# Optimization experiments

Measured on AMD Instinct MI355X. Metric: run time of the kernel, lower is better.

## Reference

```python
import jax, jax.numpy as jnp
import numpy as np

B, E, LC, LE, D = 32, 8, 256, 512, 256   # batch, evi_num, claim_len, evidence_len, emb_dim
OUT, H = 128, 1                          # attention hidden dim, head_num
NEG = -1e18


def setup_inputs() -> dict:
    key = jax.random.key(0)
    ks = jax.random.split(key, 8)
    claim = jax.random.normal(ks[0], (B, E, LC, D), jnp.float32)
    evidence = jax.random.normal(ks[1], (B, E, LE, D), jnp.float32)
    claim_len_mask = jax.random.randint(ks[2], (B, E, 1, LC), 0, 2).astype(jnp.int32)
    evidence_len_mask = jax.random.randint(ks[3], (B, E, 1, LE), 0, 2).astype(jnp.int32)
    s2d = 1.0 / np.sqrt(2 * D)
    so = 1.0 / np.sqrt(OUT)
    W1 = jax.random.normal(ks[4], (2 * D, OUT), jnp.float32) * s2d  # torch W1.weight.T
    w2 = jax.random.normal(ks[5], (OUT, H), jnp.float32) * so
    W2 = jax.random.normal(ks[6], (2 * D, OUT), jnp.float32) * s2d
    w1 = jax.random.normal(ks[7], (OUT, H), jnp.float32) * so
    return {"claim": claim, "claim_len_mask": claim_len_mask,
            "evidence": evidence, "evidence_len_mask": evidence_len_mask,
            "W1": W1, "w2": w2, "W2": W2, "w1": w1}


def _pooled_attend(seq, seq_mask, pooled, W, w):
    # seq: (B,E,L,D), pooled: (B,E,1,D), W: (2D,OUT), w: (OUT,H)
    # cat([seq, pooled_expanded]) @ W  ==  seq @ W[:D] + pooled @ W[D:]  (broadcast)
    h = jnp.tanh(seq @ W[:D] + pooled @ W[D:])          # (B,E,L,OUT)
    att = h @ w                                          # (B,E,L,H)
    mask = jnp.swapaxes(seq_mask, -1, -2).astype(bool)   # (B,E,L,1), broadcast over H
    att = jnp.where(mask, att, NEG)
    scores = jax.nn.softmax(att, axis=-2)                # softmax over L
    out = jnp.einsum('belh,beld->behd', scores, seq)     # (B,E,H,D)
    return out.reshape(out.shape[0], out.shape[1], 1, -1)  # (B,E,1,H*D)


def reference(claim, claim_len_mask, evidence, evidence_len_mask, W1, w2, W2, w1):
    c_mean = jnp.mean(claim, axis=-2, keepdims=True)     # (B,E,1,D)
    e_hat = _pooled_attend(evidence, evidence_len_mask, c_mean, W1, w2)
    e_mean = jnp.mean(evidence, axis=-2, keepdims=True)  # (B,E,1,D)
    c_hat = _pooled_attend(claim, claim_len_mask, e_mean, W2, w1)
    return c_hat, e_hat
```

## Files before the change

kernel.cpp:

```cpp
#include <hip/hip_runtime.h>
#include <hip/hip_bf16.h>
#include <math.h>

#define BE   256
#define DIM  256
#define OUTD 128
#define LCL  256
#define LEV  512
#define NEGV -1e18f

typedef short  bf16x8  __attribute__((ext_vector_type(8)));
typedef float  floatx4 __attribute__((ext_vector_type(4)));

union BF1 { __hip_bfloat16 h; unsigned short u; };
union BF2 { __hip_bfloat162 h; unsigned int u; };

__device__ __forceinline__ float fast_tanh(float x) {
    float xc = fminf(fmaxf(x, -15.f), 15.f);
    float e = __expf(2.f * xc);
    return (e - 1.f) * __builtin_amdgcn_rcpf(e + 1.f);
}

__global__ __launch_bounds__(256) void k_zero(float* __restrict__ a) {
    a[blockIdx.x * 256 + threadIdx.x] = 0.f;
}

__global__ __launch_bounds__(256) void k_pmean(
    const float* __restrict__ claim, const float* __restrict__ evidence,
    float* __restrict__ cmean, float* __restrict__ emean)
{
    const int pair = blockIdx.x;
    const int ch = blockIdx.y;
    const int t = threadIdx.x;
    const float* src;
    float* dst;
    if (ch < 8) { src = claim + ((size_t)pair * LCL + ch * 32) * DIM; dst = cmean + pair * DIM; }
    else        { src = evidence + ((size_t)pair * LEV + (ch - 8) * 32) * DIM; dst = emean + pair * DIM; }
    float s = 0.f;
#pragma unroll
    for (int r = 0; r < 32; ++r) s += src[r * DIM + t];
    unsafeAtomicAdd(&dst[t], s);
}

__global__ __launch_bounds__(256) void k_biasgemm(
    const float* __restrict__ cmean, const float* __restrict__ emean,
    const float* __restrict__ W1, const float* __restrict__ W2,
    float* __restrict__ bias_e, float* __restrict__ bias_c)
{
    const int pair = blockIdx.x;
    const int t = threadIdx.x;
    __shared__ float smc[DIM], sme[DIM];
    smc[t] = cmean[pair * DIM + t] * (1.f / LCL);
    sme[t] = emean[pair * DIM + t] * (1.f / LEV);
    __syncthreads();
    if (t < OUTD) {
        float b = 0.f;
        for (int d = 0; d < DIM; ++d) b += smc[d] * W1[(DIM + d) * OUTD + t];
        bias_e[pair * OUTD + t] = b;
    } else {
        const int o = t - OUTD;
        float b = 0.f;
        for (int d = 0; d < DIM; ++d) b += sme[d] * W2[(DIM + d) * OUTD + o];
        bias_c[pair * OUTD + o] = b;
    }
}

__global__ __launch_bounds__(256) void k_prepW(
    const float* __restrict__ W1, const float* __restrict__ W2,
    unsigned short* __restrict__ WT1, unsigned short* __restrict__ WT2)
{
    const int n = blockIdx.x;
    const float* W = blockIdx.y ? W2 : W1;
    unsigned short* WT = blockIdx.y ? WT2 : WT1;
    const int k = threadIdx.x;
    BF1 c; c.h = __float2bfloat16(W[(size_t)k * OUTD + n]);
    WT[n * DIM + k] = c.u;
}

template <int L>
__global__ __launch_bounds__(256) void k_att(
    const float* __restrict__ seq, const unsigned short* __restrict__ WT,
    const float* __restrict__ wvec, const float* __restrict__ bias,
    float* __restrict__ att)
{
    constexpr int SAPC = 136;
    __shared__ unsigned short sA[128 * SAPC];
    __shared__ float sred[128][2];

    const int pair = blockIdx.x;
    const int rowbase = blockIdx.y * 128;
    const int t = threadIdx.x;
    const int lane = t & 63;
    const int wv = t >> 6;
    const int wrow = wv >> 1, wcolg = wv & 1;
    const int q = lane >> 4, c16 = lane & 15;

    const float4* sp4 = (const float4*)(seq + ((size_t)pair * L + rowbase) * DIM);

    floatx4 acc[4][4];
#pragma unroll
    for (int ra = 0; ra < 4; ++ra)
#pragma unroll
        for (int ct = 0; ct < 4; ++ct) acc[ra][ct] = (floatx4){0.f, 0.f, 0.f, 0.f};

    const unsigned short* wbase = WT + (size_t)(wcolg * 64 + c16) * DIM + q * 8;
    bf16x8 bcur[4], bnxt[4];
#pragma unroll
    for (int ct = 0; ct < 4; ++ct)
        bcur[ct] = *(const bf16x8*)(wbase + ct * 16 * DIM);

    for (int kc = 0; kc < 2; ++kc) {
        __syncthreads();
#pragma unroll
        for (int i = 0; i < 16; ++i) {
            const int idx = t + i * 256;
            const int row = idx >> 5;
            const int f4 = idx & 31;
            const float4 v = sp4[row * 64 + kc * 32 + f4];
            BF2 lo, hi;
            lo.h = __float22bfloat162_rn(make_float2(v.x, v.y));
            hi.h = __float22bfloat162_rn(make_float2(v.z, v.w));
            *(uint2*)&sA[row * SAPC + f4 * 4] = make_uint2(lo.u, hi.u);
        }
        __syncthreads();
#pragma unroll
        for (int ks4 = 0; ks4 < 4; ++ks4) {
            const int ks = kc * 4 + ks4;
            if (ks < 7) {
#pragma unroll
                for (int ct = 0; ct < 4; ++ct)
                    bnxt[ct] = *(const bf16x8*)(wbase + ct * 16 * DIM + (ks + 1) * 32);
            }
            bf16x8 af[4];
#pragma unroll
            for (int ra = 0; ra < 4; ++ra)
                af[ra] = *(const bf16x8*)&sA[(wrow * 64 + ra * 16 + c16) * SAPC + ks4 * 32 + q * 8];
#pragma unroll
            for (int ra = 0; ra < 4; ++ra)
#pragma unroll
                for (int ct = 0; ct < 4; ++ct)
                    acc[ra][ct] = __builtin_amdgcn_mfma_f32_16x16x32_bf16(af[ra], bcur[ct], acc[ra][ct], 0, 0, 0);
#pragma unroll
            for (int ct = 0; ct < 4; ++ct) bcur[ct] = bnxt[ct];
        }
    }

    float bc[4], wc[4];
#pragma unroll
    for (int ct = 0; ct < 4; ++ct) {
        const int col = wcolg * 64 + ct * 16 + c16;
        bc[ct] = bias[pair * OUTD + col];
        wc[ct] = wvec[col];
    }
#pragma unroll
    for (int ra = 0; ra < 4; ++ra) {
#pragma unroll
        for (int reg = 0; reg < 4; ++reg) {
            float s = 0.f;
#pragma unroll
            for (int ct = 0; ct < 4; ++ct)
                s += fast_tanh(acc[ra][ct][reg] + bc[ct]) * wc[ct];
#pragma unroll
            for (int off = 1; off < 16; off <<= 1) s += __shfl_xor(s, off, 64);
            if (c16 == 0)
                sred[wrow * 64 + ra * 16 + q * 4 + reg][wcolg] = s;
        }
    }
    __syncthreads();
    if (t < 128)
        att[(size_t)pair * L + rowbase + t] = sred[t][0] + sred[t][1];
}

template <int L>
__global__ __launch_bounds__(1024) void k_soft(
    const float* __restrict__ seq, const int* __restrict__ mask,
    const float* __restrict__ att, float* __restrict__ outp)
{
    const int pair = blockIdx.x;
    const int t = threadIdx.x;
    __shared__ float p[L];
    __shared__ float red[8];
    __shared__ float red2[4][DIM];

    float lmax = -INFINITY;
    if (t < 256) {
#pragma unroll
        for (int k = 0; k < L / 256; ++k) {
            const int i = t + k * 256;
            float a = att[(size_t)pair * L + i];
            a = mask[pair * L + i] ? a : NEGV;
            p[i] = a;
            lmax = fmaxf(lmax, a);
        }
#pragma unroll
        for (int off = 32; off > 0; off >>= 1) lmax = fmaxf(lmax, __shfl_xor(lmax, off, 64));
        if ((t & 63) == 0) red[t >> 6] = lmax;
    }
    __syncthreads();
    if (t < 256) {
        const float gmax = fmaxf(fmaxf(red[0], red[1]), fmaxf(red[2], red[3]));
        float lsum = 0.f;
#pragma unroll
        for (int k = 0; k < L / 256; ++k) {
            const int i = t + k * 256;
            const float e = expf(p[i] - gmax);
            p[i] = e;
            lsum += e;
        }
#pragma unroll
        for (int off = 32; off > 0; off >>= 1) lsum += __shfl_xor(lsum, off, 64);
        if ((t & 63) == 0) red[4 + (t >> 6)] = lsum;
    }
    __syncthreads();

    const int d = t & 255, lg = t >> 8;
    constexpr int L4 = L / 4;
    const float* sp = seq + (size_t)pair * L * DIM + d;
    float o = 0.f;
    for (int l = lg * L4; l < (lg + 1) * L4; ++l) o += p[l] * sp[(size_t)l * DIM];
    red2[lg][d] = o;
    __syncthreads();
    if (t < 256) {
        const float inv = 1.f / (red[4] + red[5] + red[6] + red[7]);
        outp[pair * DIM + t] = (red2[0][t] + red2[1][t] + red2[2][t] + red2[3][t]) * inv;
    }
}

extern "C" void kernel_launch(void* const* d_in, const int* in_sizes, int n_in,
                              void* d_out, int out_size, void* d_ws, size_t ws_size,
                              hipStream_t stream) {
    const float* claim    = (const float*)d_in[0];
    const int*   cmask    = (const int*)  d_in[1];
    const float* evidence = (const float*)d_in[2];
    const int*   emask    = (const int*)  d_in[3];
    const float* W1       = (const float*)d_in[4];
    const float* w2       = (const float*)d_in[5];
    const float* W2       = (const float*)d_in[6];
    const float* w1       = (const float*)d_in[7];
    float* out = (float*)d_out;

    float* ws = (float*)d_ws;
    float* cmean  = ws;
    float* emean  = cmean + BE * DIM;
    float* bias_e = emean + BE * DIM;
    float* bias_c = bias_e + BE * OUTD;
    float* att_e  = bias_c + BE * OUTD;
    float* att_c  = att_e + BE * LEV;
    unsigned short* WT1 = (unsigned short*)(att_c + BE * LCL);
    unsigned short* WT2 = WT1 + OUTD * DIM;

    k_zero<<<512, 256, 0, stream>>>(cmean);
    k_prepW<<<dim3(128, 2), 256, 0, stream>>>(W1, W2, WT1, WT2);
    k_pmean<<<dim3(BE, 24), 256, 0, stream>>>(claim, evidence, cmean, emean);
    k_biasgemm<<<BE, 256, 0, stream>>>(cmean, emean, W1, W2, bias_e, bias_c);
    k_att<LEV><<<dim3(BE, 4), 256, 0, stream>>>(evidence, WT1, w2, bias_e, att_e);
    k_att<LCL><<<dim3(BE, 2), 256, 0, stream>>>(claim, WT2, w1, bias_c, att_c);
    k_soft<LEV><<<BE, 1024, 0, stream>>>(evidence, emask, att_e, out + BE * DIM);
    k_soft<LCL><<<BE, 1024, 0, stream>>>(claim, cmask, att_c, out);
}
```

Measured before the change: 359.1 us.

## Fuse mean/weight-prep kernels, drop atomics, vectorize softmax weighted sum

Merges the zero, weight-transpose and partial-mean kernels into one launch that writes per-chunk partial sums instead of atomically accumulating. A new reduce-and-bias kernel folds the partials and splits the bias GEMV over 512 threads. The softmax weighted-sum stage now uses float4 loads over 16 row groups with a 16-way shared reduction. Together these cut launch count and atomic traffic and widen memory accesses, at the cost of a larger partial-sum workspace.

```diff
diff --git a/kernel.cpp b/kernel.cpp
--- a/kernel.cpp
+++ b/kernel.cpp
@@ -21,60 +21,73 @@
     return (e - 1.f) * __builtin_amdgcn_rcpf(e + 1.f);
 }
 
-__global__ __launch_bounds__(256) void k_zero(float* __restrict__ a) {
-    a[blockIdx.x * 256 + threadIdx.x] = 0.f;
-}
-
-__global__ __launch_bounds__(256) void k_pmean(
+__global__ __launch_bounds__(256) void k_meanprep(
     const float* __restrict__ claim, const float* __restrict__ evidence,
-    float* __restrict__ cmean, float* __restrict__ emean)
-{
-    const int pair = blockIdx.x;
-    const int ch = blockIdx.y;
-    const int t = threadIdx.x;
-    const float* src;
-    float* dst;
-    if (ch < 8) { src = claim + ((size_t)pair * LCL + ch * 32) * DIM; dst = cmean + pair * DIM; }
-    else        { src = evidence + ((size_t)pair * LEV + (ch - 8) * 32) * DIM; dst = emean + pair * DIM; }
+    const float* __restrict__ W1, const float* __restrict__ W2,
+    float* __restrict__ partial,
+    unsigned short* __restrict__ WT1, unsigned short* __restrict__ WT2)
+{
+    const int b = blockIdx.x;
+    const int t = threadIdx.x;
+    if (b >= 3072) {
+        const int idx = b - 3072;
+        const int side = idx >> 7;
+        const int n = idx & 127;
+        const float* W = side ? W2 : W1;
+        unsigned short* WT = side ? WT2 : WT1;
+        BF1 c; c.h = __float2bfloat16(W[(size_t)t * OUTD + n]);
+        WT[n * DIM + t] = c.u;
+        return;
+    }
+    const int pair = b / 12;
+    const int chunk = b % 12;
+    const float* src = (chunk < 4)
+        ? claim + ((size_t)pair * LCL + chunk * 64) * DIM
+        : evidence + ((size_t)pair * LEV + (chunk - 4) * 64) * DIM;
     float s = 0.f;
 #pragma unroll
-    for (int r = 0; r < 32; ++r) s += src[r * DIM + t];
-    unsafeAtomicAdd(&dst[t], s);
-}
-
-__global__ __launch_bounds__(256) void k_biasgemm(
-    const float* __restrict__ cmean, const float* __restrict__ emean,
+    for (int r = 0; r < 64; ++r) s += src[r * DIM + t];
+    partial[(size_t)b * DIM + t] = s;
+}
+
+__global__ __launch_bounds__(512) void k_redbias(
+    const float* __restrict__ partial,
     const float* __restrict__ W1, const float* __restrict__ W2,
     float* __restrict__ bias_e, float* __restrict__ bias_c)
 {
     const int pair = blockIdx.x;
     const int t = threadIdx.x;
-    __shared__ float smc[DIM], sme[DIM];
-    smc[t] = cmean[pair * DIM + t] * (1.f / LCL);
-    sme[t] = emean[pair * DIM + t] * (1.f / LEV);
-    __syncthreads();
-    if (t < OUTD) {
-        float b = 0.f;
-        for (int d = 0; d < DIM; ++d) b += smc[d] * W1[(DIM + d) * OUTD + t];
-        bias_e[pair * OUTD + t] = b;
+    __shared__ float sm[2][DIM];
+    __shared__ float sb[2][2][OUTD];
+    if (t < 256) {
+        float s = 0.f;
+#pragma unroll
+        for (int j = 0; j < 4; ++j) s += partial[((size_t)pair * 12 + j) * DIM + t];
+        sm[0][t] = s * (1.f / LCL);
     } else {
-        const int o = t - OUTD;
-        float b = 0.f;
-        for (int d = 0; d < DIM; ++d) b += sme[d] * W2[(DIM + d) * OUTD + o];
-        bias_c[pair * OUTD + o] = b;
-    }
-}
-
-__global__ __launch_bounds__(256) void k_prepW(
-    const float* __restrict__ W1, const float* __restrict__ W2,
-    unsigned short* __restrict__ WT1, unsigned short* __restrict__ WT2)
-{
-    const int n = blockIdx.x;
-    const float* W = blockIdx.y ? W2 : W1;
-    unsigned short* WT = blockIdx.y ? WT2 : WT1;
-    const int k = threadIdx.x;
-    BF1 c; c.h = __float2bfloat16(W[(size_t)k * OUTD + n]);
-    WT[n * DIM + k] = c.u;
+        const int t2 = t - 256;
+        float s = 0.f;
+#pragma unroll
+        for (int j = 4; j < 12; ++j) s += partial[((size_t)pair * 12 + j) * DIM + t2];
+        sm[1][t2] = s * (1.f / LEV);
+    }
+    __syncthreads();
+    const int side = t >> 8, o = t & 127, dh = (t >> 7) & 1;
+    const float* W = side ? W2 : W1;
+    const float* m = sm[side];
+    float s = 0.f;
+#pragma unroll 8
+    for (int i = 0; i < 128; ++i) {
+        const int d = dh * 128 + i;
+        s += m[d] * W[(size_t)(DIM + d) * OUTD + o];
+    }
+    sb[side][dh][o] = s;
+    __syncthreads();
+    if (t < 256) {
+        const int sd = t >> 7, oo = t & 127;
+        const float bv = sb[sd][0][oo] + sb[sd][1][oo];
+        (sd ? bias_c : bias_e)[pair * OUTD + oo] = bv;
+    }
 }
 
 template <int L>
@@ -180,7 +193,7 @@
     const int t = threadIdx.x;
     __shared__ float p[L];
     __shared__ float red[8];
-    __shared__ float red2[4][DIM];
+    __shared__ float4 red2[16][64];
 
     float lmax = -INFINITY;
     if (t < 256) {
@@ -213,16 +226,27 @@
     }
     __syncthreads();
 
-    const int d = t & 255, lg = t >> 8;
-    constexpr int L4 = L / 4;
-    const float* sp = seq + (size_t)pair * L * DIM + d;
-    float o = 0.f;
-    for (int l = lg * L4; l < (lg + 1) * L4; ++l) o += p[l] * sp[(size_t)l * DIM];
-    red2[lg][d] = o;
-    __syncthreads();
-    if (t < 256) {
+    const int d4 = t & 63, lg = t >> 6;
+    constexpr int LC = L / 16;
+    const float4* sp4 = (const float4*)(seq + (size_t)pair * L * DIM);
+    float4 o = make_float4(0.f, 0.f, 0.f, 0.f);
+    for (int l = lg * LC; l < (lg + 1) * LC; ++l) {
+        const float pl = p[l];
+        const float4 v = sp4[l * 64 + d4];
+        o.x += pl * v.x; o.y += pl * v.y; o.z += pl * v.z; o.w += pl * v.w;
+    }
+    red2[lg][d4] = o;
+    __syncthreads();
+    if (t < 64) {
+        float4 s = make_float4(0.f, 0.f, 0.f, 0.f);
+#pragma unroll
+        for (int j = 0; j < 16; ++j) {
+            const float4 v = red2[j][t];
+            s.x += v.x; s.y += v.y; s.z += v.z; s.w += v.w;
+        }
         const float inv = 1.f / (red[4] + red[5] + red[6] + red[7]);
-        outp[pair * DIM + t] = (red2[0][t] + red2[1][t] + red2[2][t] + red2[3][t]) * inv;
+        ((float4*)(outp + (size_t)pair * DIM))[t] =
+            make_float4(s.x * inv, s.y * inv, s.z * inv, s.w * inv);
     }
 }
 
@@ -240,19 +264,16 @@
     float* out = (float*)d_out;
 
     float* ws = (float*)d_ws;
-    float* cmean  = ws;
-    float* emean  = cmean + BE * DIM;
-    float* bias_e = emean + BE * DIM;
-    float* bias_c = bias_e + BE * OUTD;
-    float* att_e  = bias_c + BE * OUTD;
-    float* att_c  = att_e + BE * LEV;
+    float* partial = ws;
+    float* bias_e  = partial + 3072 * DIM;
+    float* bias_c  = bias_e + BE * OUTD;
+    float* att_e   = bias_c + BE * OUTD;
+    float* att_c   = att_e + BE * LEV;
     unsigned short* WT1 = (unsigned short*)(att_c + BE * LCL);
     unsigned short* WT2 = WT1 + OUTD * DIM;
 
-    k_zero<<<512, 256, 0, stream>>>(cmean);
-    k_prepW<<<dim3(128, 2), 256, 0, stream>>>(W1, W2, WT1, WT2);
-    k_pmean<<<dim3(BE, 24), 256, 0, stream>>>(claim, evidence, cmean, emean);
-    k_biasgemm<<<BE, 256, 0, stream>>>(cmean, emean, W1, W2, bias_e, bias_c);
+    k_meanprep<<<3328, 256, 0, stream>>>(claim, evidence, W1, W2, partial, WT1, WT2);
+    k_redbias<<<BE, 512, 0, stream>>>(partial, W1, W2, bias_e, bias_c);
     k_att<LEV><<<dim3(BE, 4), 256, 0, stream>>>(evidence, WT1, w2, bias_e, att_e);
     k_att<LCL><<<dim3(BE, 2), 256, 0, stream>>>(claim, WT2, w1, bias_c, att_c);
     k_soft<LEV><<<BE, 1024, 0, stream>>>(evidence, emask, att_e, out + BE * DIM);
```

New measurement: 344.9 us. -4.0%, faster.
